# Performance work log

Measured on AMD Instinct MI355X. Metric: run time of the kernel, lower is better.

The kernel has to match this reference:

```python
import jax, jax.numpy as jnp
import numpy as np

TOPK, NPRO, NALP, NADS = 13, 31, 24, 37
ALPHA, BETA, EPS = 1.0, 6.0, 1e-9
BS, NA, NM = 32, 8400, 64
IMG = 640.0


def _make_boxes(key, shape, img=IMG):
    k1, k2 = jax.random.split(key)
    cxy = jax.random.uniform(k1, shape[:-1] + (2,), minval=0.0, maxval=img)
    wh = jax.random.uniform(k2, shape[:-1] + (2,), minval=10.0, maxval=120.0)
    return jnp.concatenate([cxy - wh / 2, cxy + wh / 2], axis=-1)


def setup_inputs() -> dict:
    key = jax.random.key(0)
    ks = jax.random.split(key, 12)
    pd_pro_scores = jax.random.uniform(ks[0], (BS, NA, NPRO))
    pd_alp_scores = jax.random.uniform(ks[1], (BS, NA, NALP))
    pd_ads_scores = jax.random.uniform(ks[2], (5, BS, NA, NADS))
    pd_bboxes = _make_boxes(ks[3], (BS, NA, 4))
    pd_corners = jax.random.uniform(ks[4], (BS, NA, 8), maxval=IMG)
    anc_points = jax.random.uniform(ks[5], (NA, 2), maxval=IMG)
    gt_pro = jax.random.randint(ks[6], (BS, NM, 1), 0, NPRO, dtype=jnp.int32)
    gt_alp = jax.random.randint(ks[7], (BS, NM, 1), 0, NALP, dtype=jnp.int32)
    gt_ads = jax.random.randint(ks[8], (BS, NM, 5), 0, NADS, dtype=jnp.int32)
    gt_bboxes = _make_boxes(ks[9], (BS, NM, 4))
    gt_corners = jax.random.uniform(ks[10], (BS, NM, 8), maxval=IMG)
    nvalid = jax.random.randint(ks[11], (BS,), NM // 2, NM + 1)
    mask_gt = (jnp.arange(NM)[None, :] < nvalid[:, None]).astype(jnp.float32)[..., None]
    return {"pd_pro_scores": pd_pro_scores, "pd_alp_scores": pd_alp_scores,
            "pd_ads_scores": pd_ads_scores, "pd_bboxes": pd_bboxes,
            "pd_corners": pd_corners, "anc_points": anc_points,
            "gt_pro": gt_pro, "gt_alp": gt_alp, "gt_ads": gt_ads,
            "gt_bboxes": gt_bboxes, "gt_corners": gt_corners, "mask_gt": mask_gt}


def _iou(gt, pd):
    # gt: (bs, nm, 4) xyxy; pd: (bs, na, 4) xyxy -> (bs, nm, na)
    g, p = gt[:, :, None, :], pd[:, None, :, :]
    lt = jnp.maximum(g[..., :2], p[..., :2])
    rb = jnp.minimum(g[..., 2:], p[..., 2:])
    inter = jnp.clip(rb - lt, 0).prod(-1)
    a1 = jnp.clip(g[..., 2:] - g[..., :2], 0).prod(-1)
    a2 = jnp.clip(p[..., 2:] - p[..., :2], 0).prod(-1)
    return inter / (a1 + a2 - inter + EPS)


def reference(pd_pro_scores, pd_alp_scores, pd_ads_scores, pd_bboxes, pd_corners,
              anc_points, gt_pro, gt_alp, gt_ads, gt_bboxes, gt_corners, mask_gt):
    bs, na = pd_pro_scores.shape[:2]
    nm = gt_bboxes.shape[1]
    b = jnp.arange(bs)[:, None]

    # --- get_box_metrics ---
    labels = gt_pro[..., 0].astype(jnp.int32)                       # (bs, nm)
    bbox_scores = pd_pro_scores.transpose(0, 2, 1)[b, labels]       # (bs, nm, na)
    overlaps = _iou(gt_bboxes, pd_bboxes)                           # (bs, nm, na)
    align = (bbox_scores ** ALPHA) * (overlaps ** BETA)

    # --- select_candidates_in_gts ---
    xy = anc_points[None, None]                                     # (1,1,na,2)
    d_lt = xy - gt_bboxes[:, :, None, :2]
    d_rb = gt_bboxes[:, :, None, 2:] - xy
    mask_in = (jnp.minimum(d_lt, d_rb).min(-1) > EPS).astype(align.dtype)

    # --- select_topk_candidates ---
    metrics = align * mask_in
    _, tidx = jax.lax.top_k(metrics, TOPK)                          # (bs, nm, topk)
    valid = mask_gt[..., 0] > 0                                     # (bs, nm)
    tidx = jnp.where(valid[..., None], tidx, 0)
    rows = jnp.arange(bs * nm)[:, None]
    counts = jnp.zeros((bs * nm, na), jnp.int32).at[rows, tidx.reshape(bs * nm, TOPK)].add(1)
    counts = counts.reshape(bs, nm, na)
    is_in_topk = jnp.where(counts > 1, 0, counts).astype(metrics.dtype)
    mask_pos = is_in_topk * mask_in * mask_gt                       # (bs, nm, na)

    # --- select_highest_overlaps ---
    fg_mask = mask_pos.sum(-2)                                      # (bs, na)
    multi = fg_mask > 1
    max_idx = overlaps.argmax(1)                                    # (bs, na)
    is_max = (jnp.arange(nm)[None, :, None] == max_idx[:, None, :]).astype(mask_pos.dtype)
    mask_pos = jnp.where(multi[:, None, :], is_max, mask_pos)
    fg_mask = mask_pos.sum(-2)
    target_gt_idx = mask_pos.argmax(-2)                             # (bs, na)

    # --- get_targets ---
    target_pro = jnp.maximum(gt_pro[..., 0].astype(jnp.int32)[b, target_gt_idx], 0)
    target_alp = jnp.maximum(gt_alp[..., 0].astype(jnp.int32)[b, target_gt_idx], 0)
    target_ads = jnp.maximum(gt_ads.astype(jnp.int32)[b, target_gt_idx], 0)   # (bs, na, 5)
    target_ad0_4 = jnp.moveaxis(target_ads, -1, 0)                  # (5, bs, na)
    target_bboxes = gt_bboxes[b, target_gt_idx]                     # (bs, na, 4)
    target_corners = gt_corners[b, target_gt_idx]                   # (bs, na, 8)

    fg = (fg_mask > 0).astype(jnp.float32)                          # (bs, na)
    pro_scores = jax.nn.one_hot(target_pro, NPRO, dtype=jnp.float32) * fg[..., None]
    alp_scores = jax.nn.one_hot(target_alp, NALP, dtype=jnp.float32) * fg[..., None]
    ads_scores = jax.nn.one_hot(target_ad0_4, NADS, dtype=jnp.float32) * fg[None, :, :, None]

    # --- normalization of pro scores ---
    align = align * mask_pos
    pos_align = align.max(-1, keepdims=True)                        # (bs, nm, 1)
    pos_ov = (overlaps * mask_pos).max(-1, keepdims=True)           # (bs, nm, 1)
    norm = (align * pos_ov / (pos_align + EPS)).max(-2)[..., None]  # (bs, na, 1)
    pro_scores = pro_scores * norm

    return (target_pro, target_alp, target_ad0_4, target_bboxes, target_corners,
            pro_scores, alp_scores, ads_scores, fg_mask > 0)
```

## Files before the change

kernel.cpp:

```cpp
#include <hip/hip_runtime.h>
#include <cstdint>
#include <cstddef>

#define BS 32
#define NA 8400
#define NM 64
#define NPRO 31
#define NALP 24
#define NADS 37
#define TOPK 13
#define FEPS 1e-9f
#define WORDS 264
#define CAP 512
#define TL 16
#define NFILL 4096
#define LCAP 32768

#define OFF0 0L
#define OFF1 268800L
#define OFF2 537600L
#define OFF3 1881600L
#define OFF4 2956800L
#define OFF5 5107200L
#define OFF6 13440000L
#define OFF7 19891200L
#define OFF8 69619200L
#define N4TOT 17472000L
#define S1_4  67200L
#define S2_4  134400L
#define S3_4  470400L
#define S4_4  739200L
#define Z4    1276800L

typedef float f4_t __attribute__((ext_vector_type(4)));

__device__ __forceinline__ float iou1(float4 g, float ga, float4 p, float pa) {
  float iw = fmaxf(fminf(g.z, p.z) - fmaxf(g.x, p.x), 0.f);
  float ih = fmaxf(fminf(g.w, p.w) - fmaxf(g.y, p.y), 0.f);
  float inter = iw * ih;
  return inter / (ga + pa - inter + FEPS);
}

__global__ __launch_bounds__(256) void k1(
    const float* __restrict__ pro, const float* __restrict__ pd_bb,
    const float* __restrict__ anc, const int* __restrict__ gt_pro,
    const int* __restrict__ gt_alp, const int* __restrict__ gt_ads,
    const float* __restrict__ gt_bb, const float* __restrict__ gt_cor,
    const float* __restrict__ mask_gt,
    short* __restrict__ tlist, unsigned* __restrict__ posA,
    unsigned* __restrict__ posO, int* __restrict__ gcnt,
    float* __restrict__ out)
{
  __shared__ unsigned s_in[WORDS];
  __shared__ unsigned s_pos[WORDS];
  __shared__ float s_cv[CAP];
  __shared__ int   s_ci[CAP];
  __shared__ int   s_cnt;

  const int bid = blockIdx.x;
  const int tid = threadIdx.x;

  if (bid >= BS * NM) {
    f4_t* o4 = (f4_t*)out;
    const long stride = (long)NFILL * 256;
    for (long f4 = (long)(bid - BS * NM) * 256 + tid; f4 < N4TOT; f4 += stride) {
      f4_t v;
      if (f4 >= Z4) {
        v = (f4_t){0.f, 0.f, 0.f, 0.f};
      } else if (f4 < S3_4) {
        int b; float s;
        if (f4 < S1_4) { b = (int)(f4 / 2100); s = (float)gt_pro[b * NM]; }
        else if (f4 < S2_4) { b = (int)((f4 - S1_4) / 2100); s = (float)gt_alp[b * NM]; }
        else {
          long idx = f4 - S2_4;
          int k = (int)(idx / 67200);
          int b2 = (int)(idx - (long)k * 67200) / 2100;
          b = b2; s = (float)gt_ads[b * NM * 5 + k];
        }
        v = (f4_t){s, s, s, s};
      } else if (f4 < S4_4) {
        int idx = (int)(f4 - S3_4); int b = idx / 8400;
        v = *(const f4_t*)(gt_bb + (size_t)b * NM * 4);
      } else {
        int idx = (int)(f4 - S4_4); int b = idx / 16800; int par = idx & 1;
        v = *((const f4_t*)(gt_cor + (size_t)b * NM * 8) + par);
      }
      o4[f4] = v;
    }
    return;
  }

  const int bm = bid;
  const int b = bm >> 6;
  const int lane = tid & 63;

  if (bm == 0 && tid == 0) *gcnt = 0;
  if (tid == 0) { posA[bm] = 0u; posO[bm] = 0u; s_cnt = 0; }

  short* tl = tlist + bm * TL;
  if (!(mask_gt[bm] > 0.f)) {
    if (tid == 0) tl[0] = 0;
    return;
  }
  __syncthreads();

  const float4 g = *(const float4*)(gt_bb + (size_t)bm * 4);
  const int label = gt_pro[bm];
  const float ga = fmaxf(g.z - g.x, 0.f) * fmaxf(g.w - g.y, 0.f);
  const float* pb = pd_bb + (size_t)b * NA * 4;
  const float* ps = pro + (size_t)b * NA * NPRO + label;

  for (int j = 0; j < (NA + 255) / 256; j++) {
    const int a = j * 256 + tid;
    bool inb = false, posb = false; float met = 0.f;
    if (a < NA) {
      float2 ap = *(const float2*)(anc + 2 * a);
      float din = fminf(fminf(ap.x - g.x, ap.y - g.y), fminf(g.z - ap.x, g.w - ap.y));
      if (din > FEPS) {
        inb = true;
        float4 p = *(const float4*)(pb + (size_t)a * 4);
        float pa = fmaxf(p.z - p.x, 0.f) * fmaxf(p.w - p.y, 0.f);
        float iou = iou1(g, ga, p, pa);
        float i2 = iou * iou;
        met = ps[(size_t)a * NPRO] * (i2 * i2 * i2);
        posb = met > 0.f;
      }
    }
    unsigned long long bin  = __ballot(inb);
    unsigned long long bpos = __ballot(posb);
    if (lane == 0) {
      int w0 = (j << 3) + ((tid >> 6) << 1);
      s_in[w0]      = (unsigned)bin;
      s_in[w0 + 1]  = (unsigned)(bin >> 32);
      s_pos[w0]     = (unsigned)bpos;
      s_pos[w0 + 1] = (unsigned)(bpos >> 32);
    }
    if (bpos) {
      int base = 0;
      if (lane == 0) base = atomicAdd(&s_cnt, __popcll(bpos));
      base = __shfl(base, 0);
      if (posb) {
        int idx = base + __popcll(bpos & ((1ull << lane) - 1ull));
        if (idx < CAP) { s_cv[idx] = met; s_ci[idx] = a; }
      }
    }
  }
  __syncthreads();

  const int P = min(s_cnt, CAP);
  if (tid < 64) {
    float lv[8]; int li[8];
#pragma unroll
    for (int e = 0; e < 8; e++) {
      int p = tid + e * 64;
      bool ok = p < P;
      lv[e] = ok ? s_cv[p] : -1.f;
      li[e] = ok ? s_ci[p] : NA;
    }
    const int nsel = min(P, TOPK);
    for (int k = 0; k < nsel; k++) {
      float bv = -1.f; int bi = NA;
#pragma unroll
      for (int e = 0; e < 8; e++)
        if (lv[e] > bv || (lv[e] == bv && li[e] < bi)) { bv = lv[e]; bi = li[e]; }
      for (int s = 1; s < 64; s <<= 1) {
        float ov = __shfl_xor(bv, s);
        int   oi = __shfl_xor(bi, s);
        if (ov > bv || (ov == bv && oi < bi)) { bv = ov; bi = oi; }
      }
#pragma unroll
      for (int e = 0; e < 8; e++) if (li[e] == bi) lv[e] = -1.f;
      if (tid == 0) tl[1 + k] = (short)bi;
    }
    if (tid == 0) {
      int cnt = nsel;
      if (P < TOPK) {
        int need = TOPK - P;
        for (int a = 0; a < NA && need > 0; a++) {
          if (!((s_pos[a >> 5] >> (a & 31)) & 1u)) {
            need--;
            if ((s_in[a >> 5] >> (a & 31)) & 1u) tl[1 + cnt++] = (short)a;
          }
        }
      }
      tl[0] = (short)cnt;
    }
  }
}

__global__ __launch_bounds__(256) void k2(
    const float* __restrict__ pro, const float* __restrict__ pd_bb,
    const int* __restrict__ gt_pro, const float* __restrict__ gt_bb,
    const short* __restrict__ tlist,
    unsigned* __restrict__ posA, unsigned* __restrict__ posO,
    int* __restrict__ gcnt, int* __restrict__ lpack, float* __restrict__ lav)
{
  __shared__ float4 s_g[NM];
  __shared__ float s_ga[NM];
  __shared__ int s_lab[NM];
  __shared__ unsigned long long s_m[256];
  __shared__ short s_tl[NM * TL];

  const int b = blockIdx.y;
  const int a0 = blockIdx.x << 8;
  const int tid = threadIdx.x;

  s_m[tid] = 0ull;
  if (tid < NM) {
    float4 gg = *(const float4*)(gt_bb + (size_t)(b * NM + tid) * 4);
    s_g[tid] = gg;
    s_ga[tid] = fmaxf(gg.z - gg.x, 0.f) * fmaxf(gg.w - gg.y, 0.f);
    s_lab[tid] = gt_pro[b * NM + tid];
  }
  for (int i = tid; i < NM * TL / 2; i += 256)
    ((int*)s_tl)[i] = ((const int*)(tlist + (size_t)b * NM * TL))[i];
  __syncthreads();

  for (int i = tid; i < NM * TL; i += 256) {
    int m = i >> 4, sl = i & 15;
    if (sl >= 1 && sl <= (int)s_tl[m * TL]) {
      int ai = s_tl[i];
      unsigned d = (unsigned)(ai - a0);
      if (d < 256u) atomicOr(&s_m[d], 1ull << m);
    }
  }
  __syncthreads();

  const int a = a0 + tid;
  if (a >= NA) return;

  const int ia = b * NA + a;
  unsigned long long msk = s_m[tid];
  int cnt = __popcll(msk);
  if (cnt == 0) return;

  int chosen; float ovv;
  float4 p = *(const float4*)(pd_bb + (size_t)ia * 4);
  float pa = fmaxf(p.z - p.x, 0.f) * fmaxf(p.w - p.y, 0.f);
  if (cnt == 1) {
    chosen = __ffsll(msk) - 1;
    ovv = iou1(s_g[chosen], s_ga[chosen], p, pa);
  } else {
    float best = -1.f; int bmx = 0;
    for (int m = 0; m < NM; m++) {
      float v = iou1(s_g[m], s_ga[m], p, pa);
      if (v > best) { best = v; bmx = m; }
    }
    chosen = bmx; ovv = best;
  }
  float sc = pro[(size_t)ia * NPRO + s_lab[chosen]];
  float o2 = ovv * ovv;
  float av = sc * (o2 * o2 * o2);
  atomicMax(&posA[b * NM + chosen], __float_as_uint(av));
  atomicMax(&posO[b * NM + chosen], __float_as_uint(ovv));
  int idx = atomicAdd(gcnt, 1);
  if (idx < LCAP) { lpack[idx] = ia | (chosen << 19); lav[idx] = av; }
}

__global__ __launch_bounds__(256) void k3(
    const int* __restrict__ gcnt, const int* __restrict__ lpack,
    const float* __restrict__ lav,
    const unsigned* __restrict__ posA, const unsigned* __restrict__ posO,
    const int* __restrict__ gt_pro, const int* __restrict__ gt_alp,
    const int* __restrict__ gt_ads, const float* __restrict__ gt_bb,
    const float* __restrict__ gt_cor, float* __restrict__ out)
{
  const int n = min(*gcnt, LCAP);
  const int i = blockIdx.x * 256 + threadIdx.x;
  if (i >= n) return;

  const int pk = lpack[i];
  const int ia = pk & ((1 << 19) - 1);
  const int g = pk >> 19;
  const float av = lav[i];
  const int b = ia / NA;
  const int gi = b * NM + g;

  const float no = av * __uint_as_float(posO[gi]) /
                   (__uint_as_float(posA[gi]) + FEPS);
  const int tp = gt_pro[gi], ta = gt_alp[gi];

  out[OFF0 + ia] = (float)tp;
  out[OFF1 + ia] = (float)ta;
#pragma unroll
  for (int k = 0; k < 5; k++) {
    int td = gt_ads[(size_t)gi * 5 + k];
    out[OFF2 + (size_t)k * (BS * NA) + ia] = (float)td;
    out[OFF7 + (size_t)k * ((size_t)BS * NA * NADS) + (size_t)ia * NADS + td] = 1.f;
  }
  *(float4*)(out + OFF3 + (size_t)ia * 4) = *(const float4*)(gt_bb + (size_t)gi * 4);
  *(float4*)(out + OFF4 + (size_t)ia * 8) = *(const float4*)(gt_cor + (size_t)gi * 8);
  *(float4*)(out + OFF4 + (size_t)ia * 8 + 4) = *(const float4*)(gt_cor + (size_t)gi * 8 + 4);
  out[OFF5 + (size_t)ia * NPRO + tp] = no;
  out[OFF6 + (size_t)ia * NALP + ta] = 1.f;
  out[OFF8 + ia] = 1.f;
}

extern "C" void kernel_launch(void* const* d_in, const int* in_sizes, int n_in,
                              void* d_out, int out_size, void* d_ws, size_t ws_size,
                              hipStream_t stream) {
  const float* pd_pro  = (const float*)d_in[0];
  const float* pd_bb   = (const float*)d_in[3];
  const float* anc     = (const float*)d_in[5];
  const int*   gt_pro  = (const int*)d_in[6];
  const int*   gt_alp  = (const int*)d_in[7];
  const int*   gt_ads  = (const int*)d_in[8];
  const float* gt_bb   = (const float*)d_in[9];
  const float* gt_cor  = (const float*)d_in[10];
  const float* mask_gt = (const float*)d_in[11];
  float* out = (float*)d_out;

  char* ws = (char*)d_ws;
  short*    tlist = (short*)(ws);
  unsigned* posA  = (unsigned*)(ws + 65536);
  unsigned* posO  = (unsigned*)(ws + 73728);
  int*      gcnt  = (int*)     (ws + 81920);
  int*      lpack = (int*)     (ws + 82048);
  float*    lav   = (float*)   (ws + 213120);

  k1<<<BS * NM + NFILL, 256, 0, stream>>>(pd_pro, pd_bb, anc, gt_pro, gt_alp,
                                          gt_ads, gt_bb, gt_cor, mask_gt,
                                          tlist, posA, posO, gcnt, out);
  dim3 gridB((NA + 255) / 256, BS);
  k2<<<gridB, 256, 0, stream>>>(pd_pro, pd_bb, gt_pro, gt_bb, tlist,
                                posA, posO, gcnt, lpack, lav);
  k3<<<(LCAP + 255) / 256, 256, 0, stream>>>(gcnt, lpack, lav, posA, posO,
                                             gt_pro, gt_alp, gt_ads, gt_bb,
                                             gt_cor, out);
}
```

Before: 141.2 us.

## Fuse resolve and scatter kernels into one per-batch block with shared-memory reductions

Merges k2 and k3 into a single kernel with one block per batch. Each block builds per-anchor GT masks in shared memory, resolves conflicts only for candidate anchors, keeps the pos-max reductions and the candidate list in LDS, and scatters the outputs itself. This removes a kernel launch, the global atomics and the global list round trip, and the k2 grid that covered all anchors. It also moves the fill blocks to the front of k1 and switches the fill index math to 32-bit unsigned. The trade-off is only 32 blocks doing serial per-batch work with about 70KB of shared memory each.

```diff
diff --git a/kernel.cpp b/kernel.cpp
--- a/kernel.cpp
+++ b/kernel.cpp
@@ -14,7 +14,6 @@
 #define CAP 512
 #define TL 16
 #define NFILL 4096
-#define LCAP 32768
 
 #define OFF0 0L
 #define OFF1 268800L
@@ -25,12 +24,12 @@
 #define OFF6 13440000L
 #define OFF7 19891200L
 #define OFF8 69619200L
-#define N4TOT 17472000L
-#define S1_4  67200L
-#define S2_4  134400L
-#define S3_4  470400L
-#define S4_4  739200L
-#define Z4    1276800L
+#define N4TOT 17472000u
+#define S1_4  67200u
+#define S2_4  134400u
+#define S3_4  470400u
+#define S4_4  739200u
+#define Z4    1276800u
 
 typedef float f4_t __attribute__((ext_vector_type(4)));
 
@@ -47,9 +46,7 @@
     const int* __restrict__ gt_alp, const int* __restrict__ gt_ads,
     const float* __restrict__ gt_bb, const float* __restrict__ gt_cor,
     const float* __restrict__ mask_gt,
-    short* __restrict__ tlist, unsigned* __restrict__ posA,
-    unsigned* __restrict__ posO, int* __restrict__ gcnt,
-    float* __restrict__ out)
+    short* __restrict__ tlist, float* __restrict__ out)
 {
   __shared__ unsigned s_in[WORDS];
   __shared__ unsigned s_pos[WORDS];
@@ -60,42 +57,41 @@
   const int bid = blockIdx.x;
   const int tid = threadIdx.x;
 
-  if (bid >= BS * NM) {
+  if (bid < NFILL) {
     f4_t* o4 = (f4_t*)out;
-    const long stride = (long)NFILL * 256;
-    for (long f4 = (long)(bid - BS * NM) * 256 + tid; f4 < N4TOT; f4 += stride) {
+    const unsigned stride = NFILL * 256u;
+    for (unsigned f4 = (unsigned)bid * 256u + tid; f4 < N4TOT; f4 += stride) {
       f4_t v;
       if (f4 >= Z4) {
         v = (f4_t){0.f, 0.f, 0.f, 0.f};
       } else if (f4 < S3_4) {
-        int b; float s;
-        if (f4 < S1_4) { b = (int)(f4 / 2100); s = (float)gt_pro[b * NM]; }
-        else if (f4 < S2_4) { b = (int)((f4 - S1_4) / 2100); s = (float)gt_alp[b * NM]; }
+        float s;
+        if (f4 < S1_4) { unsigned b = f4 / 2100u; s = (float)gt_pro[b * NM]; }
+        else if (f4 < S2_4) { unsigned b = (f4 - S1_4) / 2100u; s = (float)gt_alp[b * NM]; }
         else {
-          long idx = f4 - S2_4;
-          int k = (int)(idx / 67200);
-          int b2 = (int)(idx - (long)k * 67200) / 2100;
-          b = b2; s = (float)gt_ads[b * NM * 5 + k];
+          unsigned idx = f4 - S2_4;
+          unsigned k = idx / 67200u;
+          unsigned b = (idx - k * 67200u) / 2100u;
+          s = (float)gt_ads[b * NM * 5 + k];
         }
         v = (f4_t){s, s, s, s};
       } else if (f4 < S4_4) {
-        int idx = (int)(f4 - S3_4); int b = idx / 8400;
+        unsigned b = (f4 - S3_4) / 8400u;
         v = *(const f4_t*)(gt_bb + (size_t)b * NM * 4);
       } else {
-        int idx = (int)(f4 - S4_4); int b = idx / 16800; int par = idx & 1;
-        v = *((const f4_t*)(gt_cor + (size_t)b * NM * 8) + par);
+        unsigned idx = f4 - S4_4; unsigned b = idx / 16800u;
+        v = *((const f4_t*)(gt_cor + (size_t)b * NM * 8) + (idx & 1u));
       }
       o4[f4] = v;
     }
     return;
   }
 
-  const int bm = bid;
+  const int bm = bid - NFILL;
   const int b = bm >> 6;
   const int lane = tid & 63;
 
-  if (bm == 0 && tid == 0) *gcnt = 0;
-  if (tid == 0) { posA[bm] = 0u; posO[bm] = 0u; s_cnt = 0; }
+  if (tid == 0) s_cnt = 0;
 
   short* tl = tlist + bm * TL;
   if (!(mask_gt[bm] > 0.f)) {
@@ -190,110 +186,108 @@
 
 __global__ __launch_bounds__(256) void k2(
     const float* __restrict__ pro, const float* __restrict__ pd_bb,
-    const int* __restrict__ gt_pro, const float* __restrict__ gt_bb,
-    const short* __restrict__ tlist,
-    unsigned* __restrict__ posA, unsigned* __restrict__ posO,
-    int* __restrict__ gcnt, int* __restrict__ lpack, float* __restrict__ lav)
+    const int* __restrict__ gt_pro, const int* __restrict__ gt_alp,
+    const int* __restrict__ gt_ads, const float* __restrict__ gt_bb,
+    const float* __restrict__ gt_cor, const short* __restrict__ tlist,
+    float* __restrict__ out)
 {
+  __shared__ short s_tl[NM * TL];
   __shared__ float4 s_g[NM];
   __shared__ float s_ga[NM];
   __shared__ int s_lab[NM];
-  __shared__ unsigned long long s_m[256];
-  __shared__ short s_tl[NM * TL];
-
-  const int b = blockIdx.y;
-  const int a0 = blockIdx.x << 8;
+  __shared__ unsigned s_mlo[NA];
+  __shared__ unsigned s_mhi[NA];
+  __shared__ unsigned s_pA[NM], s_pO[NM];
+  __shared__ int s_la[NM * TOPK];
+  __shared__ float s_lv[NM * TOPK];
+  __shared__ int s_n;
+
+  const int b = blockIdx.x;
   const int tid = threadIdx.x;
 
-  s_m[tid] = 0ull;
+  if (tid == 0) s_n = 0;
   if (tid < NM) {
     float4 gg = *(const float4*)(gt_bb + (size_t)(b * NM + tid) * 4);
     s_g[tid] = gg;
     s_ga[tid] = fmaxf(gg.z - gg.x, 0.f) * fmaxf(gg.w - gg.y, 0.f);
     s_lab[tid] = gt_pro[b * NM + tid];
+    s_pA[tid] = 0u; s_pO[tid] = 0u;
   }
   for (int i = tid; i < NM * TL / 2; i += 256)
     ((int*)s_tl)[i] = ((const int*)(tlist + (size_t)b * NM * TL))[i];
+  for (int i = tid; i < NA; i += 256) { s_mlo[i] = 0u; s_mhi[i] = 0u; }
   __syncthreads();
 
   for (int i = tid; i < NM * TL; i += 256) {
     int m = i >> 4, sl = i & 15;
     if (sl >= 1 && sl <= (int)s_tl[m * TL]) {
-      int ai = s_tl[i];
-      unsigned d = (unsigned)(ai - a0);
-      if (d < 256u) atomicOr(&s_m[d], 1ull << m);
-    }
-  }
-  __syncthreads();
-
-  const int a = a0 + tid;
-  if (a >= NA) return;
-
-  const int ia = b * NA + a;
-  unsigned long long msk = s_m[tid];
-  int cnt = __popcll(msk);
-  if (cnt == 0) return;
-
-  int chosen; float ovv;
-  float4 p = *(const float4*)(pd_bb + (size_t)ia * 4);
-  float pa = fmaxf(p.z - p.x, 0.f) * fmaxf(p.w - p.y, 0.f);
-  if (cnt == 1) {
-    chosen = __ffsll(msk) - 1;
-    ovv = iou1(s_g[chosen], s_ga[chosen], p, pa);
-  } else {
-    float best = -1.f; int bmx = 0;
-    for (int m = 0; m < NM; m++) {
-      float v = iou1(s_g[m], s_ga[m], p, pa);
-      if (v > best) { best = v; bmx = m; }
-    }
-    chosen = bmx; ovv = best;
-  }
-  float sc = pro[(size_t)ia * NPRO + s_lab[chosen]];
-  float o2 = ovv * ovv;
-  float av = sc * (o2 * o2 * o2);
-  atomicMax(&posA[b * NM + chosen], __float_as_uint(av));
-  atomicMax(&posO[b * NM + chosen], __float_as_uint(ovv));
-  int idx = atomicAdd(gcnt, 1);
-  if (idx < LCAP) { lpack[idx] = ia | (chosen << 19); lav[idx] = av; }
-}
-
-__global__ __launch_bounds__(256) void k3(
-    const int* __restrict__ gcnt, const int* __restrict__ lpack,
-    const float* __restrict__ lav,
-    const unsigned* __restrict__ posA, const unsigned* __restrict__ posO,
-    const int* __restrict__ gt_pro, const int* __restrict__ gt_alp,
-    const int* __restrict__ gt_ads, const float* __restrict__ gt_bb,
-    const float* __restrict__ gt_cor, float* __restrict__ out)
-{
-  const int n = min(*gcnt, LCAP);
-  const int i = blockIdx.x * 256 + threadIdx.x;
-  if (i >= n) return;
-
-  const int pk = lpack[i];
-  const int ia = pk & ((1 << 19) - 1);
-  const int g = pk >> 19;
-  const float av = lav[i];
-  const int b = ia / NA;
-  const int gi = b * NM + g;
-
-  const float no = av * __uint_as_float(posO[gi]) /
-                   (__uint_as_float(posA[gi]) + FEPS);
-  const int tp = gt_pro[gi], ta = gt_alp[gi];
-
-  out[OFF0 + ia] = (float)tp;
-  out[OFF1 + ia] = (float)ta;
+      int a = s_tl[i];
+      if (m < 32) atomicOr(&s_mlo[a], 1u << m);
+      else        atomicOr(&s_mhi[a], 1u << (m - 32));
+    }
+  }
+  __syncthreads();
+
+  for (int i = tid; i < NM * TL; i += 256) {
+    int m = i >> 4, sl = i & 15;
+    if (!(sl >= 1 && sl <= (int)s_tl[m * TL])) continue;
+    int a = s_tl[i];
+    unsigned lo = s_mlo[a], hi = s_mhi[a];
+    int first = lo ? (__ffs(lo) - 1) : (31 + __ffs(hi));
+    if (m != first) continue;
+    int cnt = __popc(lo) + __popc(hi);
+
+    float4 p = *(const float4*)(pd_bb + (size_t)(b * NA + a) * 4);
+    float pa = fmaxf(p.z - p.x, 0.f) * fmaxf(p.w - p.y, 0.f);
+    int chosen; float ovv;
+    if (cnt == 1) {
+      chosen = m;
+      ovv = iou1(s_g[m], s_ga[m], p, pa);
+    } else {
+      float best = -1.f; int bmx = 0;
+      for (int mm = 0; mm < NM; mm++) {
+        float v = iou1(s_g[mm], s_ga[mm], p, pa);
+        if (v > best) { best = v; bmx = mm; }
+      }
+      chosen = bmx; ovv = best;
+    }
+    float sc = pro[(size_t)(b * NA + a) * NPRO + s_lab[chosen]];
+    float o2 = ovv * ovv;
+    float av = sc * (o2 * o2 * o2);
+    atomicMax(&s_pA[chosen], __float_as_uint(av));
+    atomicMax(&s_pO[chosen], __float_as_uint(ovv));
+    int idx = atomicAdd(&s_n, 1);
+    s_la[idx] = a | (chosen << 14);
+    s_lv[idx] = av;
+  }
+  __syncthreads();
+
+  const int n = s_n;
+  for (int j = tid; j < n; j += 256) {
+    const int a = s_la[j] & 0x3FFF;
+    const int g = s_la[j] >> 14;
+    const float av = s_lv[j];
+    const int gi = b * NM + g;
+    const int ia = b * NA + a;
+    const float no = av * __uint_as_float(s_pO[g]) /
+                     (__uint_as_float(s_pA[g]) + FEPS);
+    const int tp = gt_pro[gi], ta = gt_alp[gi];
+
+    out[OFF0 + ia] = (float)tp;
+    out[OFF1 + ia] = (float)ta;
 #pragma unroll
-  for (int k = 0; k < 5; k++) {
-    int td = gt_ads[(size_t)gi * 5 + k];
-    out[OFF2 + (size_t)k * (BS * NA) + ia] = (float)td;
-    out[OFF7 + (size_t)k * ((size_t)BS * NA * NADS) + (size_t)ia * NADS + td] = 1.f;
-  }
-  *(float4*)(out + OFF3 + (size_t)ia * 4) = *(const float4*)(gt_bb + (size_t)gi * 4);
-  *(float4*)(out + OFF4 + (size_t)ia * 8) = *(const float4*)(gt_cor + (size_t)gi * 8);
-  *(float4*)(out + OFF4 + (size_t)ia * 8 + 4) = *(const float4*)(gt_cor + (size_t)gi * 8 + 4);
-  out[OFF5 + (size_t)ia * NPRO + tp] = no;
-  out[OFF6 + (size_t)ia * NALP + ta] = 1.f;
-  out[OFF8 + ia] = 1.f;
+    for (int k = 0; k < 5; k++) {
+      int td = gt_ads[(size_t)gi * 5 + k];
+      out[OFF2 + (size_t)k * (BS * NA) + ia] = (float)td;
+      out[OFF7 + (size_t)k * ((size_t)BS * NA * NADS) + (size_t)ia * NADS + td] = 1.f;
+    }
+    *(float4*)(out + OFF3 + (size_t)ia * 4) = s_g[g];
+    *(float4*)(out + OFF4 + (size_t)ia * 8) = *(const float4*)(gt_cor + (size_t)gi * 8);
+    *(float4*)(out + OFF4 + (size_t)ia * 8 + 4) = *(const float4*)(gt_cor + (size_t)gi * 8 + 4);
+    out[OFF5 + (size_t)ia * NPRO + tp] = no;
+    out[OFF6 + (size_t)ia * NALP + ta] = 1.f;
+    out[OFF8 + ia] = 1.f;
+  }
 }
 
 extern "C" void kernel_launch(void* const* d_in, const int* in_sizes, int n_in,
@@ -310,21 +304,11 @@
   const float* mask_gt = (const float*)d_in[11];
   float* out = (float*)d_out;
 
-  char* ws = (char*)d_ws;
-  short*    tlist = (short*)(ws);
-  unsigned* posA  = (unsigned*)(ws + 65536);
-  unsigned* posO  = (unsigned*)(ws + 73728);
-  int*      gcnt  = (int*)     (ws + 81920);
-  int*      lpack = (int*)     (ws + 82048);
-  float*    lav   = (float*)   (ws + 213120);
-
-  k1<<<BS * NM + NFILL, 256, 0, stream>>>(pd_pro, pd_bb, anc, gt_pro, gt_alp,
+  short* tlist = (short*)d_ws;
+
+  k1<<<NFILL + BS * NM, 256, 0, stream>>>(pd_pro, pd_bb, anc, gt_pro, gt_alp,
                                           gt_ads, gt_bb, gt_cor, mask_gt,
-                                          tlist, posA, posO, gcnt, out);
-  dim3 gridB((NA + 255) / 256, BS);
-  k2<<<gridB, 256, 0, stream>>>(pd_pro, pd_bb, gt_pro, gt_bb, tlist,
-                                posA, posO, gcnt, lpack, lav);
-  k3<<<(LCAP + 255) / 256, 256, 0, stream>>>(gcnt, lpack, lav, posA, posO,
-                                             gt_pro, gt_alp, gt_ads, gt_bb,
-                                             gt_cor, out);
+                                          tlist, out);
+  k2<<<BS, 256, 0, stream>>>(pd_pro, pd_bb, gt_pro, gt_alp, gt_ads, gt_bb,
+                             gt_cor, tlist, out);
 }
```

Result: no change. 142.1 us (+0.7%).
